# Optimization experiments

Measured on AMD Instinct MI355X. Metric: run time of the kernel, lower is better.

## Reference

```python
import jax, jax.numpy as jnp
import numpy as np

N, E, F_IN, H, B, C = 100000, 1000000, 64, 64, 128, 10
NEG_SLOPE = 0.01   # nn.LeakyReLU default
TEMP = 0.05        # forward default temperature
EPS = 1e-16


def _gcn_norm(row, col, ew, n):
    """GCNConv symmetric normalization with added self-loops (weight 1)."""
    sl = jnp.arange(n)
    rs = jnp.concatenate([row, sl])
    cs = jnp.concatenate([col, sl])
    ws = jnp.concatenate([ew, jnp.ones((n,), ew.dtype)])
    deg = jax.ops.segment_sum(ws, cs, num_segments=n)
    dis = jnp.where(deg > 0, jax.lax.rsqrt(jnp.maximum(deg, EPS)), 0.0)
    return rs, cs, dis[rs] * ws * dis[cs]


def _gcn_conv(x, W, b, rs, cs, norm, n):
    h = x @ W                                   # [n, out]
    msg = norm[:, None] * h[rs]                 # gather + scale  [E+n, out]
    return jax.ops.segment_sum(msg, cs, num_segments=n) + b


def _smooth_max_node_weight(row, col, ew, n, t):
    """Propagate edge weights to both endpoints; per-node smooth maximum
    via temperature softmax over incident edge weights."""
    idx = jnp.concatenate([row, col])
    w = jnp.concatenate([ew, ew])
    m = jax.ops.segment_max(w, idx, num_segments=n)
    m = jnp.where(jnp.isfinite(m), m, 0.0)      # isolated nodes
    a = jnp.exp((w - m[idx]) / t)
    den = jax.ops.segment_sum(a, idx, num_segments=n)
    num = jax.ops.segment_sum(w * a, idx, num_segments=n)
    return jnp.where(den > 0, num / jnp.maximum(den, EPS), 0.0)


def setup_inputs() -> dict:
    key = jax.random.key(0)
    ks = jax.random.split(key, 12)
    x = jax.random.normal(ks[0], (N, F_IN), jnp.float32)
    edge_index = jax.random.randint(ks[1], (2, E), 0, N)
    edge_weight = jax.random.uniform(ks[2], (E,), jnp.float32)
    batch = jnp.sort(jax.random.randint(ks[3], (N,), 0, B))

    def lin(k, i, o):
        return jax.random.normal(k, (i, o), jnp.float32) / np.sqrt(i)

    return dict(
        x=x, edge_index=edge_index, edge_weight=edge_weight, batch=batch,
        W1=lin(ks[4], F_IN, H), b1=jnp.zeros((H,), jnp.float32),
        W2=lin(ks[5], H, H),    b2=jnp.zeros((H,), jnp.float32),
        W3=lin(ks[6], H, H),    b3=jnp.zeros((H,), jnp.float32),
        Wlin=lin(ks[7], 2 * H, H), blin=jnp.zeros((H,), jnp.float32),
        Wout=lin(ks[8], H, C),  bout=jnp.zeros((C,), jnp.float32),
    )


def reference(x, edge_index, edge_weight, batch,
              W1, b1, W2, b2, W3, b3, Wlin, blin, Wout, bout):
    row, col = edge_index[0], edge_index[1]
    rs, cs, norm = _gcn_norm(row, col, edge_weight, N)

    # 3-layer GCN, LeakyReLU between layers (none after last, PyG BasicGNN)
    h = jax.nn.leaky_relu(_gcn_conv(x, W1, b1, rs, cs, norm, N), NEG_SLOPE)
    h = jax.nn.leaky_relu(_gcn_conv(h, W2, b2, rs, cs, norm, N), NEG_SLOPE)
    h = _gcn_conv(h, W3, b3, rs, cs, norm, N)

    # weighted global sum / mean pooling per graph
    nw = _smooth_max_node_weight(row, col, edge_weight, N, TEMP)      # [N]
    s = jax.ops.segment_sum(h * nw[:, None], batch, num_segments=B)   # [B,H]
    wsum = jax.ops.segment_sum(nw, batch, num_segments=B)             # [B]
    mean = s / jnp.maximum(wsum, EPS)[:, None]
    feats = jnp.concatenate([s, mean], axis=1)                        # [B,2H]

    embeds = feats @ Wlin + blin          # dropout p=0 -> identity
    hout = jax.nn.relu(embeds)
    logits = hout @ Wout + bout
    probs = jax.nn.softmax(logits, axis=-1)
    return logits, probs, feats, embeds, hout
```

## Files before the change

### kernel.cpp

```cpp
#include <hip/hip_runtime.h>
#include <hip/hip_bf16.h>

typedef __hip_bfloat16 bf16;

#define NN 100000
#define NE 1000000
#define HD 64
#define NB 128
#define NC 10
#define NEG_SLOPE 0.01f
#define INV_TEMP 20.0f
#define HSTR 68
#define CAP 48

__device__ __forceinline__ float bb(unsigned short u) {
    return __uint_as_float(((unsigned)u) << 16);
}
__device__ __forceinline__ unsigned short f2bf(float f) {
    bf16 b = __float2bfloat16(f);
    union { bf16 b; unsigned short u; } cv; cv.b = b;
    return cv.u;
}
__device__ __forceinline__ float4 ld4(const float* p) { return *(const float4*)p; }
__device__ __forceinline__ float4 ld4(const bf16* p) {
    ushort4 u = *(const ushort4*)p;
    return make_float4(bb(u.x), bb(u.y), bb(u.z), bb(u.w));
}

__global__ void k_edge2(const int* __restrict__ ei, const float* __restrict__ ew,
                        int* __restrict__ cnt, int2* __restrict__ srt,
                        float* __restrict__ nm) {
    int e = blockIdx.x * 256 + threadIdx.x;
    if (e >= NE) return;
    int r = ei[e], c = ei[NE + e];
    float w = ew[e];
    int p = atomicAdd(&cnt[c], 1);
    if (p < CAP) {
        int2 pk; pk.x = r; pk.y = __float_as_int(w);
        srt[c * CAP + p] = pk;
    }
    float a = __expf(w * INV_TEMP);
    atomicAdd(&nm[2 * r], a);
    atomicAdd(&nm[2 * r + 1], w * a);
}

__global__ void k_nodeA(const int* __restrict__ cnt, const int2* __restrict__ srt,
                        const float* __restrict__ nm,
                        float* __restrict__ dis, float* __restrict__ nw,
                        const int* __restrict__ batch, int* __restrict__ gstart) {
    int i = blockIdx.x * 256 + threadIdx.x;
    if (i >= NN) return;
    {
        int b = batch[i];
        int prev = (i == 0) ? -1 : batch[i - 1];
        if (b != prev) gstart[b] = i + 1;
    }
    int n = min(cnt[i], CAP);
    int beg = i * CAP;
    float sumw = 0.f, dcol = 0.f, ncol = 0.f;
    for (int e = beg; e < beg + n; ++e) {
        float w = __int_as_float(srt[e].y);
        float a = __expf(w * INV_TEMP);
        sumw += w;
        dcol += a;
        ncol += w * a;
    }
    dis[i] = rsqrtf(sumw + 1.0f);
    float D = nm[2 * i] + dcol;
    float Nm = nm[2 * i + 1] + ncol;
    nw[i] = (D > 0.f) ? Nm / fmaxf(D, 1e-16f) : 0.f;
}

#define GROW(h, A0, A1, A2, A3)                                               \
    A0 += h.x * w0.x; A1 += h.x * w0.y; A2 += h.x * w0.z; A3 += h.x * w0.w;   \
    A0 += h.y * w1.x; A1 += h.y * w1.y; A2 += h.y * w1.z; A3 += h.y * w1.w;   \
    A0 += h.z * w2.x; A1 += h.z * w2.y; A2 += h.z * w2.z; A3 += h.z * w2.w;   \
    A0 += h.w * w3.x; A1 += h.w * w3.y; A2 += h.w * w3.z; A3 += h.w * w3.w;

template <typename TIN>
__global__ __launch_bounds__(256, 2)
void k_gemm(const TIN* __restrict__ Hin, const float* __restrict__ W,
            bf16* __restrict__ T) {
    __shared__ float Hs[64 * HSTR];
    __shared__ float Ws[64 * 64];
    int tid = threadIdx.x;
    int row0 = blockIdx.x * 64;
    {
        const float4* W4 = (const float4*)W;
        float4* Ws4 = (float4*)Ws;
#pragma unroll
        for (int i = 0; i < 4; ++i) Ws4[tid + i * 256] = W4[tid + i * 256];
    }
#pragma unroll
    for (int i = 0; i < 4; ++i) {
        int idx = tid + i * 256;
        int r = idx >> 4, k4 = idx & 15;
        int row = row0 + r;
        float4 v = make_float4(0.f, 0.f, 0.f, 0.f);
        if (row < NN) v = ld4(Hin + (size_t)row * HD + 4 * k4);
        *(float4*)(&Hs[r * HSTR + 4 * k4]) = v;
    }
    __syncthreads();
    int tc = tid & 15, tr = tid >> 4;
    float a00 = 0.f, a01 = 0.f, a02 = 0.f, a03 = 0.f;
    float a10 = 0.f, a11 = 0.f, a12 = 0.f, a13 = 0.f;
    float a20 = 0.f, a21 = 0.f, a22 = 0.f, a23 = 0.f;
    float a30 = 0.f, a31 = 0.f, a32 = 0.f, a33 = 0.f;
#pragma unroll 2
    for (int kk = 0; kk < 16; ++kk) {
        float4 h0 = *(const float4*)(&Hs[(4 * tr + 0) * HSTR + 4 * kk]);
        float4 h1 = *(const float4*)(&Hs[(4 * tr + 1) * HSTR + 4 * kk]);
        float4 h2 = *(const float4*)(&Hs[(4 * tr + 2) * HSTR + 4 * kk]);
        float4 h3 = *(const float4*)(&Hs[(4 * tr + 3) * HSTR + 4 * kk]);
        float4 w0 = *(const float4*)(&Ws[(4 * kk + 0) * 64 + 4 * tc]);
        float4 w1 = *(const float4*)(&Ws[(4 * kk + 1) * 64 + 4 * tc]);
        float4 w2 = *(const float4*)(&Ws[(4 * kk + 2) * 64 + 4 * tc]);
        float4 w3 = *(const float4*)(&Ws[(4 * kk + 3) * 64 + 4 * tc]);
        GROW(h0, a00, a01, a02, a03)
        GROW(h1, a10, a11, a12, a13)
        GROW(h2, a20, a21, a22, a23)
        GROW(h3, a30, a31, a32, a33)
    }
    unsigned short* Tu = (unsigned short*)T;
    int row;
    row = row0 + 4 * tr + 0;
    if (row < NN) { ushort4 o; o.x = f2bf(a00); o.y = f2bf(a01); o.z = f2bf(a02); o.w = f2bf(a03);
                    *(ushort4*)(Tu + (size_t)row * HD + 4 * tc) = o; }
    row = row0 + 4 * tr + 1;
    if (row < NN) { ushort4 o; o.x = f2bf(a10); o.y = f2bf(a11); o.z = f2bf(a12); o.w = f2bf(a13);
                    *(ushort4*)(Tu + (size_t)row * HD + 4 * tc) = o; }
    row = row0 + 4 * tr + 2;
    if (row < NN) { ushort4 o; o.x = f2bf(a20); o.y = f2bf(a21); o.z = f2bf(a22); o.w = f2bf(a23);
                    *(ushort4*)(Tu + (size_t)row * HD + 4 * tc) = o; }
    row = row0 + 4 * tr + 3;
    if (row < NN) { ushort4 o; o.x = f2bf(a30); o.y = f2bf(a31); o.z = f2bf(a32); o.w = f2bf(a33);
                    *(ushort4*)(Tu + (size_t)row * HD + 4 * tc) = o; }
}

template <int FIXN, int OBF>
__global__ void k_agg(const bf16* __restrict__ T, const int* __restrict__ cnt,
                      int2* __restrict__ srt,
                      const float* __restrict__ dis, const float* __restrict__ bias,
                      void* __restrict__ Hout, int lrelu) {
    int wv = threadIdx.x >> 6, lane = threadIdx.x & 63;
    int grp = lane >> 4, fl = lane & 15;
    int node = blockIdx.x * 4 + wv;
    if (node >= NN) return;
    float d = dis[node];
    float a0 = 0.f, a1 = 0.f, a2 = 0.f, a3 = 0.f;
    if (grp == 0) {
        ushort4 tv = *(const ushort4*)(T + (size_t)node * HD + 4 * fl);
        a0 = d * bb(tv.x); a1 = d * bb(tv.y); a2 = d * bb(tv.z); a3 = d * bb(tv.w);
    }
    int beg = node * CAP, end = beg + min(cnt[node], CAP);
    for (int e0 = beg; e0 < end; e0 += 4) {
        int e = e0 + grp;
        if (e < end) {
            int2 p = srt[e];
            float pw;
            if (FIXN) {
                pw = dis[p.x] * __int_as_float(p.y);
                if (fl == 0) ((float*)srt)[2 * e + 1] = pw;
            } else {
                pw = __int_as_float(p.y);
            }
            ushort4 tv = *(const ushort4*)(T + (size_t)p.x * HD + 4 * fl);
            a0 += pw * bb(tv.x);
            a1 += pw * bb(tv.y);
            a2 += pw * bb(tv.z);
            a3 += pw * bb(tv.w);
        }
    }
    a0 += __shfl_xor(a0, 16, 64); a1 += __shfl_xor(a1, 16, 64);
    a2 += __shfl_xor(a2, 16, 64); a3 += __shfl_xor(a3, 16, 64);
    a0 += __shfl_xor(a0, 32, 64); a1 += __shfl_xor(a1, 32, 64);
    a2 += __shfl_xor(a2, 32, 64); a3 += __shfl_xor(a3, 32, 64);
    if (lane < 16) {
        float4 bv = *(const float4*)(bias + 4 * lane);
        float4 o;
        o.x = bv.x + d * a0;
        o.y = bv.y + d * a1;
        o.z = bv.z + d * a2;
        o.w = bv.w + d * a3;
        if (lrelu) {
            o.x = o.x > 0.f ? o.x : NEG_SLOPE * o.x;
            o.y = o.y > 0.f ? o.y : NEG_SLOPE * o.y;
            o.z = o.z > 0.f ? o.z : NEG_SLOPE * o.z;
            o.w = o.w > 0.f ? o.w : NEG_SLOPE * o.w;
        }
        if (OBF) {
            ushort4 u; u.x = f2bf(o.x); u.y = f2bf(o.y); u.z = f2bf(o.z); u.w = f2bf(o.w);
            *(ushort4*)((unsigned short*)Hout + (size_t)node * HD + 4 * lane) = u;
        } else {
            *(float4*)((float*)Hout + (size_t)node * HD + 4 * lane) = o;
        }
    }
}

__global__ void k_poolmlp(const float* __restrict__ H3, const float* __restrict__ nw,
                          const int* __restrict__ gstart,
                          const float* __restrict__ Wlin, const float* __restrict__ blin,
                          const float* __restrict__ Wout, const float* __restrict__ bout,
                          float* __restrict__ out) {
    __shared__ float sred[4][64];
    __shared__ float wred[4];
    __shared__ float wsum_s;
    __shared__ int sbeg, send;
    __shared__ float fs[128];
    __shared__ float hs[64];
    __shared__ float lg[10];
    int b = blockIdx.x, t = threadIdx.x;
    if (t == 0) {
        int mn = NN;
        for (int j = NB; j > b; --j) {
            int g = gstart[j];
            int v = (g == 0) ? NN : g - 1;
            mn = min(mn, v);
        }
        send = mn;
        int g = gstart[b];
        int v = (g == 0) ? NN : g - 1;
        sbeg = min(mn, v);
    }
    __syncthreads();
    int wv = t >> 6, lane = t & 63;
    float accs = 0.f, accw = 0.f;
    for (int n = sbeg + wv; n < send; n += 4) {
        float wn = nw[n];
        accs += wn * H3[n * HD + lane];
        accw += wn;
    }
    sred[wv][lane] = accs;
    if (lane == 0) wred[wv] = accw;
    __syncthreads();
    if (t < 64) {
        float s = sred[0][lane] + sred[1][lane] + sred[2][lane] + sred[3][lane];
        if (lane == 0) wsum_s = wred[0] + wred[1] + wred[2] + wred[3];
        fs[lane] = s;
        out[2560 + b * 128 + lane] = s;
    }
    __syncthreads();
    if (t < 64) {
        float mean = fs[lane] / fmaxf(wsum_s, 1e-16f);
        fs[64 + lane] = mean;
        out[2560 + b * 128 + 64 + lane] = mean;
    }
    __syncthreads();
    if (t < 64) {
        float acc = blin[t];
        for (int k = 0; k < 128; ++k) acc += fs[k] * Wlin[k * 64 + t];
        out[18944 + b * 64 + t] = acc;
        float h = fmaxf(acc, 0.f);
        out[27136 + b * 64 + t] = h;
        hs[t] = h;
    }
    __syncthreads();
    if (t < NC) {
        float acc = bout[t];
        for (int j = 0; j < 64; ++j) acc += hs[j] * Wout[j * NC + t];
        lg[t] = acc;
        out[b * NC + t] = acc;
    }
    __syncthreads();
    if (t < NC) {
        float mx = lg[0];
        for (int k = 1; k < NC; ++k) mx = fmaxf(mx, lg[k]);
        float se = 0.f;
        for (int k = 0; k < NC; ++k) se += __expf(lg[k] - mx);
        float p = __expf(lg[t] - mx) / se;
        out[1280 + b * NC + t] = p;
    }
}

extern "C" void kernel_launch(void* const* d_in, const int* in_sizes, int n_in,
                              void* d_out, int out_size, void* d_ws, size_t ws_size,
                              hipStream_t stream) {
    const float* x    = (const float*)d_in[0];
    const int*   ei   = (const int*)  d_in[1];
    const float* ew   = (const float*)d_in[2];
    const int*   batch= (const int*)  d_in[3];
    const float* W1   = (const float*)d_in[4];
    const float* b1   = (const float*)d_in[5];
    const float* W2   = (const float*)d_in[6];
    const float* b2   = (const float*)d_in[7];
    const float* W3   = (const float*)d_in[8];
    const float* b3   = (const float*)d_in[9];
    const float* Wlin = (const float*)d_in[10];
    const float* blin = (const float*)d_in[11];
    const float* Wout = (const float*)d_in[12];
    const float* bout = (const float*)d_in[13];
    float* out = (float*)d_out;

    char* ws = (char*)d_ws;
    size_t off = 0;
    auto alloc = [&](size_t bytes) -> void* {
        void* p = ws + off;
        off = (off + bytes + 255) & ~(size_t)255;
        return p;
    };
    int*   cnt  = (int*)  alloc(NN * 4);
    float* nm   = (float*)alloc((size_t)NN * 2 * 4);
    int* gstart = (int*)  alloc((NB + 1) * 4);
    size_t zbytes = off;
    float* dis    = (float*)alloc(NN * 4);
    float* nw     = (float*)alloc(NN * 4);
    int2* srt     = (int2*) alloc((size_t)NN * CAP * 8);
    bf16* Tbuf    = (bf16*) alloc((size_t)NN * HD * 2);
    bf16* Hbf     = (bf16*) alloc((size_t)NN * HD * 2);
    float* Hbuf   = (float*)alloc((size_t)NN * HD * 4);
    (void)ws_size; (void)in_sizes; (void)n_in; (void)out_size;

    const int EB = (NE + 255) / 256;
    const int VB = (NN + 255) / 256;
    const int GB = (NN + 63) / 64;

    hipMemsetAsync(ws, 0, zbytes, stream);
    k_edge2<<<EB, 256, 0, stream>>>(ei, ew, cnt, srt, nm);
    k_nodeA<<<VB, 256, 0, stream>>>(cnt, srt, nm, dis, nw, batch, gstart);

    k_gemm<float><<<GB, 256, 0, stream>>>(x, W1, Tbuf);
    k_agg<1, 1><<<NN / 4, 256, 0, stream>>>(Tbuf, cnt, srt, dis, b1, Hbf, 1);
    k_gemm<bf16><<<GB, 256, 0, stream>>>(Hbf, W2, Tbuf);
    k_agg<0, 1><<<NN / 4, 256, 0, stream>>>(Tbuf, cnt, srt, dis, b2, Hbf, 1);
    k_gemm<bf16><<<GB, 256, 0, stream>>>(Hbf, W3, Tbuf);
    k_agg<0, 0><<<NN / 4, 256, 0, stream>>>(Tbuf, cnt, srt, dis, b3, Hbuf, 0);

    k_poolmlp<<<NB, 256, 0, stream>>>(Hbuf, nw, gstart, Wlin, blin, Wout, bout, out);
}
```

Baseline: 519.9 us.

## Fuse GCN aggregation with next layer's GEMM via shared-memory tile

Layers 1 and 2 now run aggregation, bias and LeakyReLU inside the same block that then multiplies by the next weight matrix. The aggregated rows sit in shared memory instead of a bf16 intermediate in global memory. This removes two kernel launches and the write and re-read of the intermediate activations, and it drops one bf16 rounding step. In exchange, each block of 64 nodes processes its aggregation serially, 16 nodes per wave, and the 2-blocks-per-CU launch bound may limit how much gather latency is hidden.

Result: slower. 604.7 us (+16.3%).

```diff
diff --git a/kernel.cpp b/kernel.cpp
--- a/kernel.cpp
+++ b/kernel.cpp
@@ -77,30 +77,8 @@
     A0 += h.z * w2.x; A1 += h.z * w2.y; A2 += h.z * w2.z; A3 += h.z * w2.w;   \
     A0 += h.w * w3.x; A1 += h.w * w3.y; A2 += h.w * w3.z; A3 += h.w * w3.w;
 
-template <typename TIN>
-__global__ __launch_bounds__(256, 2)
-void k_gemm(const TIN* __restrict__ Hin, const float* __restrict__ W,
-            bf16* __restrict__ T) {
-    __shared__ float Hs[64 * HSTR];
-    __shared__ float Ws[64 * 64];
-    int tid = threadIdx.x;
-    int row0 = blockIdx.x * 64;
-    {
-        const float4* W4 = (const float4*)W;
-        float4* Ws4 = (float4*)Ws;
-#pragma unroll
-        for (int i = 0; i < 4; ++i) Ws4[tid + i * 256] = W4[tid + i * 256];
-    }
-#pragma unroll
-    for (int i = 0; i < 4; ++i) {
-        int idx = tid + i * 256;
-        int r = idx >> 4, k4 = idx & 15;
-        int row = row0 + r;
-        float4 v = make_float4(0.f, 0.f, 0.f, 0.f);
-        if (row < NN) v = ld4(Hin + (size_t)row * HD + 4 * k4);
-        *(float4*)(&Hs[r * HSTR + 4 * k4]) = v;
-    }
-    __syncthreads();
+__device__ __forceinline__ void gemm_core(const float* Hs, const float* Ws,
+                                          int tid, int row0, bf16* Tout) {
     int tc = tid & 15, tr = tid >> 4;
     float a00 = 0.f, a01 = 0.f, a02 = 0.f, a03 = 0.f;
     float a10 = 0.f, a11 = 0.f, a12 = 0.f, a13 = 0.f;
@@ -121,7 +99,7 @@
         GROW(h2, a20, a21, a22, a23)
         GROW(h3, a30, a31, a32, a33)
     }
-    unsigned short* Tu = (unsigned short*)T;
+    unsigned short* Tu = (unsigned short*)Tout;
     int row;
     row = row0 + 4 * tr + 0;
     if (row < NN) { ushort4 o; o.x = f2bf(a00); o.y = f2bf(a01); o.z = f2bf(a02); o.w = f2bf(a03);
@@ -137,11 +115,110 @@
                     *(ushort4*)(Tu + (size_t)row * HD + 4 * tc) = o; }
 }
 
-template <int FIXN, int OBF>
-__global__ void k_agg(const bf16* __restrict__ T, const int* __restrict__ cnt,
-                      int2* __restrict__ srt,
-                      const float* __restrict__ dis, const float* __restrict__ bias,
-                      void* __restrict__ Hout, int lrelu) {
+__global__ __launch_bounds__(256, 2)
+void k_gemm(const float* __restrict__ Hin, const float* __restrict__ W,
+            bf16* __restrict__ T) {
+    __shared__ float Hs[64 * HSTR];
+    __shared__ float Ws[64 * 64];
+    int tid = threadIdx.x;
+    int row0 = blockIdx.x * 64;
+    {
+        const float4* W4 = (const float4*)W;
+        float4* Ws4 = (float4*)Ws;
+#pragma unroll
+        for (int i = 0; i < 4; ++i) Ws4[tid + i * 256] = W4[tid + i * 256];
+    }
+#pragma unroll
+    for (int i = 0; i < 4; ++i) {
+        int idx = tid + i * 256;
+        int r = idx >> 4, k4 = idx & 15;
+        int row = row0 + r;
+        float4 v = make_float4(0.f, 0.f, 0.f, 0.f);
+        if (row < NN) v = ld4(Hin + (size_t)row * HD + 4 * k4);
+        *(float4*)(&Hs[r * HSTR + 4 * k4]) = v;
+    }
+    __syncthreads();
+    gemm_core(Hs, Ws, tid, row0, T);
+}
+
+template <int FIXN>
+__global__ __launch_bounds__(256, 2)
+void k_agggemm(const bf16* __restrict__ T, const int* __restrict__ cnt,
+               int2* __restrict__ srt, const float* __restrict__ dis,
+               const float* __restrict__ bias, const float* __restrict__ W,
+               bf16* __restrict__ Tout) {
+    __shared__ float Hs[64 * HSTR];
+    __shared__ float Ws[64 * 64];
+    int tid = threadIdx.x;
+    int wv = tid >> 6, lane = tid & 63;
+    int grp = lane >> 4, fl = lane & 15;
+    int row0 = blockIdx.x * 64;
+    {
+        const float4* W4 = (const float4*)W;
+        float4* Ws4 = (float4*)Ws;
+#pragma unroll
+        for (int i = 0; i < 4; ++i) Ws4[tid + i * 256] = W4[tid + i * 256];
+    }
+    for (int j = 0; j < 16; ++j) {
+        int rloc = wv * 16 + j;
+        int node = row0 + rloc;
+        float a0 = 0.f, a1 = 0.f, a2 = 0.f, a3 = 0.f;
+        float d = 0.f;
+        if (node < NN) {
+            d = dis[node];
+            if (grp == 0) {
+                ushort4 tv = *(const ushort4*)(T + (size_t)node * HD + 4 * fl);
+                a0 = d * bb(tv.x); a1 = d * bb(tv.y);
+                a2 = d * bb(tv.z); a3 = d * bb(tv.w);
+            }
+            int beg = node * CAP, end = beg + min(cnt[node], CAP);
+            for (int e0 = beg; e0 < end; e0 += 4) {
+                int e = e0 + grp;
+                if (e < end) {
+                    int2 p = srt[e];
+                    float pw;
+                    if (FIXN) {
+                        pw = dis[p.x] * __int_as_float(p.y);
+                        if (fl == 0) ((float*)srt)[2 * e + 1] = pw;
+                    } else {
+                        pw = __int_as_float(p.y);
+                    }
+                    ushort4 tv = *(const ushort4*)(T + (size_t)p.x * HD + 4 * fl);
+                    a0 += pw * bb(tv.x);
+                    a1 += pw * bb(tv.y);
+                    a2 += pw * bb(tv.z);
+                    a3 += pw * bb(tv.w);
+                }
+            }
+        }
+        a0 += __shfl_xor(a0, 16, 64); a1 += __shfl_xor(a1, 16, 64);
+        a2 += __shfl_xor(a2, 16, 64); a3 += __shfl_xor(a3, 16, 64);
+        a0 += __shfl_xor(a0, 32, 64); a1 += __shfl_xor(a1, 32, 64);
+        a2 += __shfl_xor(a2, 32, 64); a3 += __shfl_xor(a3, 32, 64);
+        if (lane < 16) {
+            float4 o = make_float4(0.f, 0.f, 0.f, 0.f);
+            if (node < NN) {
+                float4 bv = *(const float4*)(bias + 4 * lane);
+                o.x = bv.x + d * a0;
+                o.y = bv.y + d * a1;
+                o.z = bv.z + d * a2;
+                o.w = bv.w + d * a3;
+                o.x = o.x > 0.f ? o.x : NEG_SLOPE * o.x;
+                o.y = o.y > 0.f ? o.y : NEG_SLOPE * o.y;
+                o.z = o.z > 0.f ? o.z : NEG_SLOPE * o.z;
+                o.w = o.w > 0.f ? o.w : NEG_SLOPE * o.w;
+            }
+            *(float4*)(&Hs[rloc * HSTR + 4 * lane]) = o;
+        }
+    }
+    __syncthreads();
+    gemm_core(Hs, Ws, tid, row0, Tout);
+}
+
+__global__ void k_agg3(const bf16* __restrict__ T, const int* __restrict__ cnt,
+                       const int2* __restrict__ srt,
+                       const float* __restrict__ dis, const float* __restrict__ bias,
+                       float* __restrict__ Hout) {
     int wv = threadIdx.x >> 6, lane = threadIdx.x & 63;
     int grp = lane >> 4, fl = lane & 15;
     int node = blockIdx.x * 4 + wv;
@@ -157,13 +234,7 @@
         int e = e0 + grp;
         if (e < end) {
             int2 p = srt[e];
-            float pw;
-            if (FIXN) {
-                pw = dis[p.x] * __int_as_float(p.y);
-                if (fl == 0) ((float*)srt)[2 * e + 1] = pw;
-            } else {
-                pw = __int_as_float(p.y);
-            }
+            float pw = __int_as_float(p.y);
             ushort4 tv = *(const ushort4*)(T + (size_t)p.x * HD + 4 * fl);
             a0 += pw * bb(tv.x);
             a1 += pw * bb(tv.y);
@@ -182,18 +253,7 @@
         o.y = bv.y + d * a1;
         o.z = bv.z + d * a2;
         o.w = bv.w + d * a3;
-        if (lrelu) {
-            o.x = o.x > 0.f ? o.x : NEG_SLOPE * o.x;
-            o.y = o.y > 0.f ? o.y : NEG_SLOPE * o.y;
-            o.z = o.z > 0.f ? o.z : NEG_SLOPE * o.z;
-            o.w = o.w > 0.f ? o.w : NEG_SLOPE * o.w;
-        }
-        if (OBF) {
-            ushort4 u; u.x = f2bf(o.x); u.y = f2bf(o.y); u.z = f2bf(o.z); u.w = f2bf(o.w);
-            *(ushort4*)((unsigned short*)Hout + (size_t)node * HD + 4 * lane) = u;
-        } else {
-            *(float4*)((float*)Hout + (size_t)node * HD + 4 * lane) = o;
-        }
+        *(float4*)(Hout + (size_t)node * HD + 4 * lane) = o;
     }
 }
 
@@ -306,7 +366,7 @@
     float* nw     = (float*)alloc(NN * 4);
     int2* srt     = (int2*) alloc((size_t)NN * CAP * 8);
     bf16* Tbuf    = (bf16*) alloc((size_t)NN * HD * 2);
-    bf16* Hbf     = (bf16*) alloc((size_t)NN * HD * 2);
+    bf16* Tbuf2   = (bf16*) alloc((size_t)NN * HD * 2);
     float* Hbuf   = (float*)alloc((size_t)NN * HD * 4);
     (void)ws_size; (void)in_sizes; (void)n_in; (void)out_size;
 
@@ -318,12 +378,10 @@
     k_edge2<<<EB, 256, 0, stream>>>(ei, ew, cnt, srt, nm);
     k_nodeA<<<VB, 256, 0, stream>>>(cnt, srt, nm, dis, nw, batch, gstart);
 
-    k_gemm<float><<<GB, 256, 0, stream>>>(x, W1, Tbuf);
-    k_agg<1, 1><<<NN / 4, 256, 0, stream>>>(Tbuf, cnt, srt, dis, b1, Hbf, 1);
-    k_gemm<bf16><<<GB, 256, 0, stream>>>(Hbf, W2, Tbuf);
-    k_agg<0, 1><<<NN / 4, 256, 0, stream>>>(Tbuf, cnt, srt, dis, b2, Hbf, 1);
-    k_gemm<bf16><<<GB, 256, 0, stream>>>(Hbf, W3, Tbuf);
-    k_agg<0, 0><<<NN / 4, 256, 0, stream>>>(Tbuf, cnt, srt, dis, b3, Hbuf, 0);
+    k_gemm<<<GB, 256, 0, stream>>>(x, W1, Tbuf);
+    k_agggemm<1><<<GB, 256, 0, stream>>>(Tbuf, cnt, srt, dis, b1, W2, Tbuf2);
+    k_agggemm<0><<<GB, 256, 0, stream>>>(Tbuf2, cnt, srt, dis, b2, W3, Tbuf);
+    k_agg3<<<NN / 4, 256, 0, stream>>>(Tbuf, cnt, srt, dis, b3, Hbuf);
 
     k_poolmlp<<<NB, 256, 0, stream>>>(Hbuf, nw, gstart, Wlin, blin, Wout, bout, out);
 }
```
